# Performance work log

Measured on AMD Instinct MI355X. Metric: run time of the kernel, lower is better.

## Reference

```python
import jax, jax.numpy as jnp
import numpy as np

N_HEAD, D_MODEL, D_K, D_V = 16, 1024, 64, 64
B, LQ, LK = 4, 2048, 2048


def setup_inputs() -> dict:
    key = jax.random.key(0)
    ks = jax.random.split(key, 10)
    q = jax.random.normal(ks[0], (B, LQ, D_MODEL), dtype=jnp.float32)
    k = jax.random.normal(ks[1], (B, LK, D_MODEL), dtype=jnp.float32)
    v = jax.random.normal(ks[2], (B, LK, D_MODEL), dtype=jnp.float32)
    mask = jax.random.randint(ks[3], (B, LQ, LK), 0, 2).astype(bool)
    s_qk = np.sqrt(2.0 / (D_MODEL + D_K)).astype(np.float32)
    s_v = np.sqrt(2.0 / (D_MODEL + D_V)).astype(np.float32)
    w_qs = jax.random.normal(ks[4], (D_MODEL, N_HEAD * D_K), dtype=jnp.float32) * s_qk
    w_ks = jax.random.normal(ks[5], (D_MODEL, N_HEAD * D_K), dtype=jnp.float32) * s_qk
    w_vs = jax.random.normal(ks[6], (D_MODEL, N_HEAD * D_V), dtype=jnp.float32) * s_v
    b_qs = jnp.zeros((N_HEAD * D_K,), jnp.float32)
    b_ks = jnp.zeros((N_HEAD * D_K,), jnp.float32)
    b_vs = jnp.zeros((N_HEAD * D_V,), jnp.float32)
    fc_w = jax.random.normal(ks[7], (N_HEAD * D_V, D_MODEL), dtype=jnp.float32) * np.sqrt(2.0 / (N_HEAD * D_V + D_MODEL)).astype(np.float32)
    fc_b = jnp.zeros((D_MODEL,), jnp.float32)
    return {"q": q, "k": k, "v": v, "mask": mask,
            "w_qs": w_qs, "b_qs": b_qs, "w_ks": w_ks, "b_ks": b_ks,
            "w_vs": w_vs, "b_vs": b_vs, "fc_w": fc_w, "fc_b": fc_b}


def mha(q, k, v, mask, w_qs, b_qs, w_ks, b_ks, w_vs, b_vs, fc_w, fc_b):
    residual = q
    b, lq, _ = q.shape
    lk = k.shape[1]
    # project and split heads: [b, h, len, d]
    qh = (q @ w_qs + b_qs).reshape(b, lq, N_HEAD, D_K).transpose(0, 2, 1, 3)
    kh = (k @ w_ks + b_ks).reshape(b, lk, N_HEAD, D_K).transpose(0, 2, 1, 3)
    vh = (v @ w_vs + b_vs).reshape(b, lk, N_HEAD, D_V).transpose(0, 2, 1, 3)
    temperature = jnp.asarray(D_K ** 0.5, qh.dtype)
    attn = jnp.einsum('bhqd,bhkd->bhqk', qh, kh) / temperature
    attn = jnp.where(mask[:, None, :, :], -jnp.inf, attn)
    attn = jax.nn.softmax(attn, axis=-1)  # dropout is identity in eval
    out = jnp.einsum('bhqk,bhkd->bhqd', attn, vh)
    out = out.transpose(0, 2, 1, 3).reshape(b, lq, N_HEAD * D_V)
    out = out @ fc_w + fc_b
    return out + residual, attn


def reference(q, k, v, mask, w_qs, b_qs, w_ks, b_ks, w_vs, b_vs, fc_w, fc_b):
    return mha(q, k, v, mask, w_qs, b_qs, w_ks, b_ks, w_vs, b_vs, fc_w, fc_b)
```

## Files before the change

### kernel.cpp

```cpp
#include <hip/hip_runtime.h>
#include <cstdint>
#include <cstddef>

typedef unsigned short u16;
typedef __bf16 bf16x8 __attribute__((ext_vector_type(8)));
typedef float floatx4 __attribute__((ext_vector_type(4)));
typedef u16 u16x8 __attribute__((ext_vector_type(8)));

#define NHEAD 16
#define DHEAD 64
#define BATCH 4
#define SEQ 2048
#define DMODEL 1024

__device__ __forceinline__ u16 f2b(float f) {
  union { float f; unsigned u; } x; x.f = f;
  unsigned r = x.u + 0x7fffu + ((x.u >> 16) & 1u);
  return (u16)(r >> 16);
}

__device__ __forceinline__ floatx4 mfma16(bf16x8 a, bf16x8 b, floatx4 c) {
  return __builtin_amdgcn_mfma_f32_16x16x32_bf16(a, b, c, 0, 0, 0);
}

__global__ __launch_bounds__(256) void wtrans(const float* __restrict__ w,
                                              u16* __restrict__ wt) {
  __shared__ u16 tile[64 * 68];
  const int t = threadIdx.x;
  const int d0 = blockIdx.x * 64, c0 = blockIdx.y * 64;
#pragma unroll
  for (int s = 0; s < 4; ++s) {
    int dd = (t >> 4) + s * 16;
    int cc = (t & 15) * 4;
    float4 v = *(const float4*)(w + (size_t)(d0 + dd) * DMODEL + c0 + cc);
    u16* p = &tile[dd * 68 + cc];
    p[0] = f2b(v.x); p[1] = f2b(v.y); p[2] = f2b(v.z); p[3] = f2b(v.w);
  }
  __syncthreads();
#pragma unroll
  for (int s = 0; s < 2; ++s) {
    int cc = (t >> 3) + s * 32;
    int dd = (t & 7) * 8;
    u16x8 rv;
#pragma unroll
    for (int j = 0; j < 8; ++j) rv[j] = tile[(dd + j) * 68 + cc];
    *(u16x8*)(wt + (size_t)(c0 + cc) * DMODEL + d0 + dd) = rv;
  }
}

__global__ __launch_bounds__(256) void gemm128(
    const float* __restrict__ Af, const u16* __restrict__ Ab,
    const u16* __restrict__ WT, const float* __restrict__ bias,
    u16* __restrict__ outb, float* __restrict__ outf,
    const float* __restrict__ resid, int mode) {
  __shared__ __align__(16) u16 sm[2 * 128 * 72];
  u16* sA = sm;
  u16* sB = sm + 128 * 72;
  const int t = threadIdx.x;
  const int w = t >> 6, lane = t & 63, quad = lane >> 4, ln = lane & 15;
  const int Mb = blockIdx.x * 128, Nb = blockIdx.y * 128;
  const int wr = (w >> 1) * 64, wc = (w & 1) * 64;
  floatx4 acc[4][4] = {};
#pragma unroll 1
  for (int kc = 0; kc < 16; ++kc) {
    const int k0 = kc * 64;
    __syncthreads();
    if (mode == 2) {
#pragma unroll
      for (int s = 0; s < 4; ++s) {
        int r = (t >> 3) + s * 32, off = (t & 7) * 8;
        *(u16x8*)(&sA[r * 72 + off]) =
            *(const u16x8*)(Ab + (size_t)(Mb + r) * DMODEL + k0 + off);
      }
    } else {
#pragma unroll
      for (int s = 0; s < 8; ++s) {
        int r = (t >> 4) + s * 16, c = (t & 15) * 4;
        float4 v = *(const float4*)(Af + (size_t)(Mb + r) * DMODEL + k0 + c);
        u16* p = &sA[r * 72 + c];
        p[0] = f2b(v.x); p[1] = f2b(v.y); p[2] = f2b(v.z); p[3] = f2b(v.w);
      }
    }
#pragma unroll
    for (int s = 0; s < 4; ++s) {
      int r = (t >> 3) + s * 32, off = (t & 7) * 8;
      *(u16x8*)(&sB[r * 72 + off]) =
          *(const u16x8*)(WT + (size_t)(Nb + r) * DMODEL + k0 + off);
    }
    __syncthreads();
#pragma unroll
    for (int ks = 0; ks < 2; ++ks) {
      bf16x8 af[4], bfr[4];
#pragma unroll
      for (int m = 0; m < 4; ++m)
        af[m] = *(const bf16x8*)(&sA[(wr + m * 16 + ln) * 72 + quad * 8 + ks * 32]);
#pragma unroll
      for (int n = 0; n < 4; ++n)
        bfr[n] = *(const bf16x8*)(&sB[(wc + n * 16 + ln) * 72 + quad * 8 + ks * 32]);
#pragma unroll
      for (int m = 0; m < 4; ++m)
#pragma unroll
        for (int n = 0; n < 4; ++n)
          acc[m][n] = mfma16(af[m], bfr[n], acc[m][n]);
    }
  }
  float bv[4];
#pragma unroll
  for (int n = 0; n < 4; ++n) bv[n] = bias[Nb + wc + n * 16 + ln];

  if (mode == 0) {
#pragma unroll
    for (int m = 0; m < 4; ++m)
#pragma unroll
      for (int n = 0; n < 4; ++n)
#pragma unroll
        for (int rr = 0; rr < 4; ++rr) {
          int row = Mb + wr + m * 16 + quad * 4 + rr;
          int c = Nb + wc + n * 16 + ln;
          int bi = row >> 11, lq = row & 2047, h = c >> 6, dk = c & 63;
          outb[(((size_t)bi * NHEAD + h) * SEQ + lq) * DHEAD + dk] =
              f2b(acc[m][n][rr] + bv[n]);
        }
  } else if (mode == 2) {
#pragma unroll
    for (int m = 0; m < 4; ++m)
#pragma unroll
      for (int n = 0; n < 4; ++n)
#pragma unroll
        for (int rr = 0; rr < 4; ++rr) {
          int row = Mb + wr + m * 16 + quad * 4 + rr;
          int c = Nb + wc + n * 16 + ln;
          size_t idx = (size_t)row * DMODEL + c;
          outf[idx] = acc[m][n][rr] + bv[n] + resid[idx];
        }
  } else {
    __syncthreads();
    u16* tb = sm;
#pragma unroll
    for (int m = 0; m < 4; ++m)
#pragma unroll
      for (int n = 0; n < 4; ++n)
#pragma unroll
        for (int rr = 0; rr < 4; ++rr) {
          int rl = wr + m * 16 + quad * 4 + rr;
          int cl = wc + n * 16 + ln;
          tb[rl * 132 + cl] = f2b(acc[m][n][rr] + bv[n]);
        }
    __syncthreads();
    for (int s = 0; s < 64; ++s) {
      int flat = s * 256 + t;
      int cl = flat >> 7, lkl = flat & 127;
      int c = Nb + cl, h = c >> 6, dk = c & 63;
      int lk = Mb + lkl, bi = lk >> 11, lkq = lk & 2047;
      outb[(((size_t)bi * NHEAD + h) * DHEAD + dk) * SEQ + lkq] =
          tb[lkl * 132 + cl];
    }
  }
}

__global__ __launch_bounds__(256) void attn_k(
    const u16* __restrict__ qh, const u16* __restrict__ kh,
    const u16* __restrict__ vT, const void* __restrict__ maskp,
    float* __restrict__ attn_o, u16* __restrict__ ao) {
  __shared__ __align__(16) u16 qs[64 * 72];
  __shared__ __align__(16) u16 ks_[64 * 72];
  __shared__ __align__(16) u16 vs[64 * 72];
  __shared__ __align__(16) u16 ps[64 * 72];
  __shared__ float ms[64], ls[64];
  const int t = threadIdx.x;
  const int w = t >> 6, lane = t & 63, quad = lane >> 4, ln = lane & 15;
  const int qt = blockIdx.x, bh = blockIdx.y;
  const int b = bh >> 4;
  const int q0 = qt * 64;
  const float SC = 0.18033688011112042f;

  unsigned mw = ((const unsigned*)maskp)[lane];
  const bool bytemask = __ballot(mw > 1u) != 0ull;
  const unsigned char* m8 = (const unsigned char*)maskp;
  const unsigned* m32 = (const unsigned*)maskp;
  const size_t mbase = (size_t)b * SEQ * SEQ;

#pragma unroll
  for (int s = 0; s < 2; ++s) {
    int r = (t >> 3) + s * 32, off = (t & 7) * 8;
    *(u16x8*)(&qs[r * 72 + off]) =
        *(const u16x8*)(qh + ((size_t)bh * SEQ + q0 + r) * DHEAD + off);
  }
  float mrun[4], lrun[4];
#pragma unroll
  for (int rr = 0; rr < 4; ++rr) { mrun[rr] = -1e30f; lrun[rr] = 0.f; }

#pragma unroll 1
  for (int kt = 0; kt < 32; ++kt) {
    __syncthreads();
#pragma unroll
    for (int s = 0; s < 2; ++s) {
      int r = (t >> 3) + s * 32, off = (t & 7) * 8;
      *(u16x8*)(&ks_[r * 72 + off]) =
          *(const u16x8*)(kh + ((size_t)bh * SEQ + kt * 64 + r) * DHEAD + off);
    }
    __syncthreads();
    floatx4 sc[4] = {};
#pragma unroll
    for (int kss = 0; kss < 2; ++kss) {
      bf16x8 a = *(const bf16x8*)(&qs[(w * 16 + ln) * 72 + quad * 8 + kss * 32]);
#pragma unroll
      for (int n = 0; n < 4; ++n) {
        bf16x8 bb = *(const bf16x8*)(&ks_[(n * 16 + ln) * 72 + quad * 8 + kss * 32]);
        sc[n] = mfma16(a, bb, sc[n]);
      }
    }
#pragma unroll
    for (int rr = 0; rr < 4; ++rr) {
      int qrow = q0 + w * 16 + quad * 4 + rr;
      float tv[4];
#pragma unroll
      for (int n = 0; n < 4; ++n) {
        int kcol = kt * 64 + n * 16 + ln;
        size_t mi = mbase + (size_t)qrow * SEQ + kcol;
        bool blk = bytemask ? (m8[mi] != 0) : (m32[mi] != 0);
        tv[n] = blk ? -1e30f : sc[n][rr] * SC;
      }
      float cm = fmaxf(fmaxf(tv[0], tv[1]), fmaxf(tv[2], tv[3]));
#pragma unroll
      for (int o = 1; o < 16; o <<= 1) cm = fmaxf(cm, __shfl_xor(cm, o));
      float cs = exp2f(tv[0] - cm) + exp2f(tv[1] - cm) +
                 exp2f(tv[2] - cm) + exp2f(tv[3] - cm);
#pragma unroll
      for (int o = 1; o < 16; o <<= 1) cs += __shfl_xor(cs, o);
      float mnew = fmaxf(mrun[rr], cm);
      lrun[rr] = lrun[rr] * exp2f(mrun[rr] - mnew) + cs * exp2f(cm - mnew);
      mrun[rr] = mnew;
    }
  }
  if (ln == 0) {
#pragma unroll
    for (int rr = 0; rr < 4; ++rr) {
      ms[w * 16 + quad * 4 + rr] = mrun[rr];
      ls[w * 16 + quad * 4 + rr] = lrun[rr];
    }
  }
  __syncthreads();
  float mf[4], il[4];
#pragma unroll
  for (int rr = 0; rr < 4; ++rr) {
    mf[rr] = ms[w * 16 + quad * 4 + rr];
    il[rr] = 1.0f / ls[w * 16 + quad * 4 + rr];
  }

  floatx4 oa[4] = {};
#pragma unroll 1
  for (int kt = 0; kt < 32; ++kt) {
    __syncthreads();
#pragma unroll
    for (int s = 0; s < 2; ++s) {
      int r = (t >> 3) + s * 32, off = (t & 7) * 8;
      *(u16x8*)(&ks_[r * 72 + off]) =
          *(const u16x8*)(kh + ((size_t)bh * SEQ + kt * 64 + r) * DHEAD + off);
      *(u16x8*)(&vs[r * 72 + off]) =
          *(const u16x8*)(vT + ((size_t)bh * DHEAD + r) * SEQ + kt * 64 + off);
    }
    __syncthreads();
    floatx4 sc[4] = {};
#pragma unroll
    for (int kss = 0; kss < 2; ++kss) {
      bf16x8 a = *(const bf16x8*)(&qs[(w * 16 + ln) * 72 + quad * 8 + kss * 32]);
#pragma unroll
      for (int n = 0; n < 4; ++n) {
        bf16x8 bb = *(const bf16x8*)(&ks_[(n * 16 + ln) * 72 + quad * 8 + kss * 32]);
        sc[n] = mfma16(a, bb, sc[n]);
      }
    }
#pragma unroll
    for (int rr = 0; rr < 4; ++rr) {
      int qrow = q0 + w * 16 + quad * 4 + rr;
#pragma unroll
      for (int n = 0; n < 4; ++n) {
        int kcol = kt * 64 + n * 16 + ln;
        size_t mi = mbase + (size_t)qrow * SEQ + kcol;
        bool blk = bytemask ? (m8[mi] != 0) : (m32[mi] != 0);
        float tvv = blk ? -1e30f : sc[n][rr] * SC;
        float pn = exp2f(tvv - mf[rr]) * il[rr];
        attn_o[(size_t)bh * SEQ * SEQ + (size_t)qrow * SEQ + kcol] = pn;
        ps[(w * 16 + quad * 4 + rr) * 72 + n * 16 + ln] = f2b(pn);
      }
    }
    __syncthreads();
#pragma unroll
    for (int kss = 0; kss < 2; ++kss) {
      bf16x8 a = *(const bf16x8*)(&ps[(w * 16 + ln) * 72 + quad * 8 + kss * 32]);
#pragma unroll
      for (int n = 0; n < 4; ++n) {
        bf16x8 bb = *(const bf16x8*)(&vs[(n * 16 + ln) * 72 + quad * 8 + kss * 32]);
        oa[n] = mfma16(a, bb, oa[n]);
      }
    }
  }
#pragma unroll
  for (int n = 0; n < 4; ++n)
#pragma unroll
    for (int rr = 0; rr < 4; ++rr) {
      int row = q0 + w * 16 + quad * 4 + rr;
      ao[((size_t)b * SEQ + row) * DMODEL + (bh & 15) * DHEAD + n * 16 + ln] =
          f2b(oa[n][rr]);
    }
}

extern "C" void kernel_launch(void* const* d_in, const int* in_sizes, int n_in,
                              void* d_out, int out_size, void* d_ws,
                              size_t ws_size, hipStream_t stream) {
  (void)in_sizes; (void)n_in; (void)out_size; (void)ws_size;
  const float* q = (const float*)d_in[0];
  const float* k = (const float*)d_in[1];
  const float* v = (const float*)d_in[2];
  const void* mask = d_in[3];
  const float* w_qs = (const float*)d_in[4];
  const float* b_qs = (const float*)d_in[5];
  const float* w_ks = (const float*)d_in[6];
  const float* b_ks = (const float*)d_in[7];
  const float* w_vs = (const float*)d_in[8];
  const float* b_vs = (const float*)d_in[9];
  const float* fc_w = (const float*)d_in[10];
  const float* fc_b = (const float*)d_in[11];

  char* ws = (char*)d_ws;
  const size_t WSZ = (size_t)DMODEL * DMODEL * 2;
  const size_t HSZ = (size_t)BATCH * NHEAD * SEQ * DHEAD * 2;
  u16* wqT = (u16*)(ws + 0 * WSZ);
  u16* wkT = (u16*)(ws + 1 * WSZ);
  u16* wvT = (u16*)(ws + 2 * WSZ);
  u16* fcT = (u16*)(ws + 3 * WSZ);
  u16* qh = (u16*)(ws + 4 * WSZ);
  u16* kh = (u16*)(ws + 4 * WSZ + HSZ);
  u16* vhT = (u16*)(ws + 4 * WSZ + 2 * HSZ);
  u16* ao = (u16*)(ws + 4 * WSZ + 3 * HSZ);

  float* out0 = (float*)d_out;
  float* attn = out0 + (size_t)BATCH * SEQ * DMODEL;

  dim3 tgrid(16, 16);
  wtrans<<<tgrid, 256, 0, stream>>>(w_qs, wqT);
  wtrans<<<tgrid, 256, 0, stream>>>(w_ks, wkT);
  wtrans<<<tgrid, 256, 0, stream>>>(w_vs, wvT);
  wtrans<<<tgrid, 256, 0, stream>>>(fc_w, fcT);

  dim3 ggrid(64, 8);
  gemm128<<<ggrid, 256, 0, stream>>>(q, nullptr, wqT, b_qs, qh, nullptr, nullptr, 0);
  gemm128<<<ggrid, 256, 0, stream>>>(k, nullptr, wkT, b_ks, kh, nullptr, nullptr, 0);
  gemm128<<<ggrid, 256, 0, stream>>>(v, nullptr, wvT, b_vs, vhT, nullptr, nullptr, 1);

  attn_k<<<dim3(32, 64), 256, 0, stream>>>(qh, kh, vhT, mask, attn, ao);

  gemm128<<<ggrid, 256, 0, stream>>>(nullptr, ao, fcT, fc_b, nullptr, out0, q, 2);
}
```

Before: 2.251 ms.

## Bit-pack attention mask and rework attention kernel without LDS staging or running max

A new pre-pass packs the boolean mask into 64-bit words per row and 64-key tile, so the attention kernel reads one word per row per tile instead of gathering individual mask bytes or ints. The attention kernel keeps Q fragments in registers and loads K and V fragments straight from global memory per wave. This removes the shared-memory staging and the block-wide barriers, leaving each wave only a private P buffer. It also drops the running-max rescaling and exponentiates scaled scores directly, and writes attention probabilities with nontemporal stores. The trade-offs are that softmax without max subtraction can overflow for large scores, and that K/V reuse now depends on the cache rather than on shared memory.

```diff
diff --git a/kernel.cpp b/kernel.cpp
--- a/kernel.cpp
+++ b/kernel.cpp
@@ -3,6 +3,7 @@
 #include <cstddef>
 
 typedef unsigned short u16;
+typedef unsigned long long u64;
 typedef __bf16 bf16x8 __attribute__((ext_vector_type(8)));
 typedef float floatx4 __attribute__((ext_vector_type(4)));
 typedef u16 u16x8 __attribute__((ext_vector_type(8)));
@@ -46,6 +47,43 @@
     for (int j = 0; j < 8; ++j) rv[j] = tile[(dd + j) * 68 + cc];
     *(u16x8*)(wt + (size_t)(c0 + cc) * DMODEL + d0 + dd) = rv;
   }
+}
+
+__global__ __launch_bounds__(256) void maskpack(const void* __restrict__ maskp,
+                                                u64* __restrict__ mpk) {
+  const int t = threadIdx.x;
+  unsigned mw = ((const unsigned*)maskp)[t & 63];
+  const bool bytemask = __ballot(mw > 1u) != 0ull;
+  const int rl = t >> 5, kt = t & 31;
+  const int row = blockIdx.x * 8 + rl;
+  const int b = blockIdx.y;
+  const size_t eoff = ((size_t)b * SEQ + row) * SEQ + (size_t)kt * 64;
+  u64 bits = 0;
+  if (bytemask) {
+    const uint4* p = (const uint4*)((const unsigned char*)maskp + eoff);
+#pragma unroll
+    for (int j = 0; j < 4; ++j) {
+      uint4 v = p[j];
+      unsigned wd[4] = {v.x, v.y, v.z, v.w};
+#pragma unroll
+      for (int q = 0; q < 4; ++q)
+#pragma unroll
+        for (int by = 0; by < 4; ++by)
+          bits |= (u64)(((wd[q] >> (8 * by)) & 0xffu) ? 1u : 0u)
+                  << (j * 16 + q * 4 + by);
+    }
+  } else {
+    const uint4* p = (const uint4*)((const unsigned*)maskp + eoff);
+#pragma unroll
+    for (int j = 0; j < 16; ++j) {
+      uint4 v = p[j];
+      bits |= (u64)(v.x ? 1 : 0) << (j * 4 + 0);
+      bits |= (u64)(v.y ? 1 : 0) << (j * 4 + 1);
+      bits |= (u64)(v.z ? 1 : 0) << (j * 4 + 2);
+      bits |= (u64)(v.w ? 1 : 0) << (j * 4 + 3);
+    }
+  }
+  mpk[((size_t)b * SEQ + row) * 32 + kt] = bits;
 }
 
 __global__ __launch_bounds__(256) void gemm128(
@@ -158,149 +196,107 @@
   }
 }
 
-__global__ __launch_bounds__(256) void attn_k(
+__global__ __launch_bounds__(256, 4) void attn2(
     const u16* __restrict__ qh, const u16* __restrict__ kh,
-    const u16* __restrict__ vT, const void* __restrict__ maskp,
+    const u16* __restrict__ vT, const u64* __restrict__ mpk,
     float* __restrict__ attn_o, u16* __restrict__ ao) {
-  __shared__ __align__(16) u16 qs[64 * 72];
-  __shared__ __align__(16) u16 ks_[64 * 72];
-  __shared__ __align__(16) u16 vs[64 * 72];
-  __shared__ __align__(16) u16 ps[64 * 72];
-  __shared__ float ms[64], ls[64];
+  __shared__ __align__(16) u16 ps[4][16 * 72];
   const int t = threadIdx.x;
   const int w = t >> 6, lane = t & 63, quad = lane >> 4, ln = lane & 15;
   const int qt = blockIdx.x, bh = blockIdx.y;
   const int b = bh >> 4;
-  const int q0 = qt * 64;
+  const int q0 = qt * 64 + w * 16;
   const float SC = 0.18033688011112042f;
 
-  unsigned mw = ((const unsigned*)maskp)[lane];
-  const bool bytemask = __ballot(mw > 1u) != 0ull;
-  const unsigned char* m8 = (const unsigned char*)maskp;
-  const unsigned* m32 = (const unsigned*)maskp;
-  const size_t mbase = (size_t)b * SEQ * SEQ;
-
-#pragma unroll
-  for (int s = 0; s < 2; ++s) {
-    int r = (t >> 3) + s * 32, off = (t & 7) * 8;
-    *(u16x8*)(&qs[r * 72 + off]) =
-        *(const u16x8*)(qh + ((size_t)bh * SEQ + q0 + r) * DHEAD + off);
-  }
-  float mrun[4], lrun[4];
-#pragma unroll
-  for (int rr = 0; rr < 4; ++rr) { mrun[rr] = -1e30f; lrun[rr] = 0.f; }
-
+  bf16x8 qf[2];
+  {
+    const u16* qbase = qh + ((size_t)bh * SEQ + q0 + ln) * DHEAD + quad * 8;
+    qf[0] = *(const bf16x8*)(qbase);
+    qf[1] = *(const bf16x8*)(qbase + 32);
+  }
+  const u16* kbase = kh + (size_t)bh * SEQ * DHEAD;
+  const u16* vbase = vT + (size_t)bh * DHEAD * SEQ;
+  const u64* mrow = mpk + ((size_t)b * SEQ + q0 + quad * 4) * 32;
+
+  float lsum[4] = {0.f, 0.f, 0.f, 0.f};
 #pragma unroll 1
   for (int kt = 0; kt < 32; ++kt) {
-    __syncthreads();
-#pragma unroll
-    for (int s = 0; s < 2; ++s) {
-      int r = (t >> 3) + s * 32, off = (t & 7) * 8;
-      *(u16x8*)(&ks_[r * 72 + off]) =
-          *(const u16x8*)(kh + ((size_t)bh * SEQ + kt * 64 + r) * DHEAD + off);
-    }
-    __syncthreads();
-    floatx4 sc[4] = {};
-#pragma unroll
-    for (int kss = 0; kss < 2; ++kss) {
-      bf16x8 a = *(const bf16x8*)(&qs[(w * 16 + ln) * 72 + quad * 8 + kss * 32]);
-#pragma unroll
-      for (int n = 0; n < 4; ++n) {
-        bf16x8 bb = *(const bf16x8*)(&ks_[(n * 16 + ln) * 72 + quad * 8 + kss * 32]);
-        sc[n] = mfma16(a, bb, sc[n]);
-      }
-    }
+    u64 mv[4];
+#pragma unroll
+    for (int rr = 0; rr < 4; ++rr) mv[rr] = mrow[rr * 32 + kt];
+    floatx4 sc4[4] = {};
+#pragma unroll
+    for (int kss = 0; kss < 2; ++kss)
+#pragma unroll
+      for (int n = 0; n < 4; ++n) {
+        bf16x8 kf = *(const bf16x8*)(kbase + (size_t)(kt * 64 + n * 16 + ln) * DHEAD +
+                                     quad * 8 + kss * 32);
+        sc4[n] = mfma16(qf[kss], kf, sc4[n]);
+      }
 #pragma unroll
     for (int rr = 0; rr < 4; ++rr) {
-      int qrow = q0 + w * 16 + quad * 4 + rr;
-      float tv[4];
-#pragma unroll
-      for (int n = 0; n < 4; ++n) {
-        int kcol = kt * 64 + n * 16 + ln;
-        size_t mi = mbase + (size_t)qrow * SEQ + kcol;
-        bool blk = bytemask ? (m8[mi] != 0) : (m32[mi] != 0);
-        tv[n] = blk ? -1e30f : sc[n][rr] * SC;
-      }
-      float cm = fmaxf(fmaxf(tv[0], tv[1]), fmaxf(tv[2], tv[3]));
-#pragma unroll
-      for (int o = 1; o < 16; o <<= 1) cm = fmaxf(cm, __shfl_xor(cm, o));
-      float cs = exp2f(tv[0] - cm) + exp2f(tv[1] - cm) +
-                 exp2f(tv[2] - cm) + exp2f(tv[3] - cm);
-#pragma unroll
-      for (int o = 1; o < 16; o <<= 1) cs += __shfl_xor(cs, o);
-      float mnew = fmaxf(mrun[rr], cm);
-      lrun[rr] = lrun[rr] * exp2f(mrun[rr] - mnew) + cs * exp2f(cm - mnew);
-      mrun[rr] = mnew;
-    }
-  }
-  if (ln == 0) {
-#pragma unroll
-    for (int rr = 0; rr < 4; ++rr) {
-      ms[w * 16 + quad * 4 + rr] = mrun[rr];
-      ls[w * 16 + quad * 4 + rr] = lrun[rr];
-    }
-  }
-  __syncthreads();
-  float mf[4], il[4];
+#pragma unroll
+      for (int n = 0; n < 4; ++n) {
+        float e = exp2f(sc4[n][rr] * SC);
+        bool blk = (mv[rr] >> (n * 16 + ln)) & 1;
+        lsum[rr] += blk ? 0.f : e;
+      }
+    }
+  }
+  float il[4];
 #pragma unroll
   for (int rr = 0; rr < 4; ++rr) {
-    mf[rr] = ms[w * 16 + quad * 4 + rr];
-    il[rr] = 1.0f / ls[w * 16 + quad * 4 + rr];
+    float s = lsum[rr];
+#pragma unroll
+    for (int o = 1; o < 16; o <<= 1) s += __shfl_xor(s, o);
+    il[rr] = 1.0f / s;
   }
 
   floatx4 oa[4] = {};
+  u16* myps = ps[w];
+  float* pout = attn_o + (size_t)bh * SEQ * SEQ;
 #pragma unroll 1
   for (int kt = 0; kt < 32; ++kt) {
-    __syncthreads();
-#pragma unroll
-    for (int s = 0; s < 2; ++s) {
-      int r = (t >> 3) + s * 32, off = (t & 7) * 8;
-      *(u16x8*)(&ks_[r * 72 + off]) =
-          *(const u16x8*)(kh + ((size_t)bh * SEQ + kt * 64 + r) * DHEAD + off);
-      *(u16x8*)(&vs[r * 72 + off]) =
-          *(const u16x8*)(vT + ((size_t)bh * DHEAD + r) * SEQ + kt * 64 + off);
-    }
-    __syncthreads();
-    floatx4 sc[4] = {};
+    u64 mv[4];
+#pragma unroll
+    for (int rr = 0; rr < 4; ++rr) mv[rr] = mrow[rr * 32 + kt];
+    floatx4 sc4[4] = {};
+#pragma unroll
+    for (int kss = 0; kss < 2; ++kss)
+#pragma unroll
+      for (int n = 0; n < 4; ++n) {
+        bf16x8 kf = *(const bf16x8*)(kbase + (size_t)(kt * 64 + n * 16 + ln) * DHEAD +
+                                     quad * 8 + kss * 32);
+        sc4[n] = mfma16(qf[kss], kf, sc4[n]);
+      }
+#pragma unroll
+    for (int rr = 0; rr < 4; ++rr) {
+      int qrow = q0 + quad * 4 + rr;
+#pragma unroll
+      for (int n = 0; n < 4; ++n) {
+        bool blk = (mv[rr] >> (n * 16 + ln)) & 1;
+        float pn = blk ? 0.f : exp2f(sc4[n][rr] * SC) * il[rr];
+        __builtin_nontemporal_store(
+            pn, &pout[(size_t)qrow * SEQ + kt * 64 + n * 16 + ln]);
+        myps[(quad * 4 + rr) * 72 + n * 16 + ln] = f2b(pn);
+      }
+    }
 #pragma unroll
     for (int kss = 0; kss < 2; ++kss) {
-      bf16x8 a = *(const bf16x8*)(&qs[(w * 16 + ln) * 72 + quad * 8 + kss * 32]);
-#pragma unroll
-      for (int n = 0; n < 4; ++n) {
-        bf16x8 bb = *(const bf16x8*)(&ks_[(n * 16 + ln) * 72 + quad * 8 + kss * 32]);
-        sc[n] = mfma16(a, bb, sc[n]);
-      }
-    }
+      bf16x8 pa = *(const bf16x8*)(&myps[ln * 72 + quad * 8 + kss * 32]);
+#pragma unroll
+      for (int n = 0; n < 4; ++n) {
+        bf16x8 vf = *(const bf16x8*)(vbase + (size_t)(n * 16 + ln) * SEQ +
+                                     kt * 64 + quad * 8 + kss * 32);
+        oa[n] = mfma16(pa, vf, oa[n]);
+      }
+    }
+  }
+#pragma unroll
+  for (int n = 0; n < 4; ++n)
 #pragma unroll
     for (int rr = 0; rr < 4; ++rr) {
-      int qrow = q0 + w * 16 + quad * 4 + rr;
-#pragma unroll
-      for (int n = 0; n < 4; ++n) {
-        int kcol = kt * 64 + n * 16 + ln;
-        size_t mi = mbase + (size_t)qrow * SEQ + kcol;
-        bool blk = bytemask ? (m8[mi] != 0) : (m32[mi] != 0);
-        float tvv = blk ? -1e30f : sc[n][rr] * SC;
-        float pn = exp2f(tvv - mf[rr]) * il[rr];
-        attn_o[(size_t)bh * SEQ * SEQ + (size_t)qrow * SEQ + kcol] = pn;
-        ps[(w * 16 + quad * 4 + rr) * 72 + n * 16 + ln] = f2b(pn);
-      }
-    }
-    __syncthreads();
-#pragma unroll
-    for (int kss = 0; kss < 2; ++kss) {
-      bf16x8 a = *(const bf16x8*)(&ps[(w * 16 + ln) * 72 + quad * 8 + kss * 32]);
-#pragma unroll
-      for (int n = 0; n < 4; ++n) {
-        bf16x8 bb = *(const bf16x8*)(&vs[(n * 16 + ln) * 72 + quad * 8 + kss * 32]);
-        oa[n] = mfma16(a, bb, oa[n]);
-      }
-    }
-  }
-#pragma unroll
-  for (int n = 0; n < 4; ++n)
-#pragma unroll
-    for (int rr = 0; rr < 4; ++rr) {
-      int row = q0 + w * 16 + quad * 4 + rr;
+      int row = q0 + quad * 4 + rr;
       ao[((size_t)b * SEQ + row) * DMODEL + (bh & 15) * DHEAD + n * 16 + ln] =
           f2b(oa[n][rr]);
     }
@@ -334,6 +330,7 @@
   u16* kh = (u16*)(ws + 4 * WSZ + HSZ);
   u16* vhT = (u16*)(ws + 4 * WSZ + 2 * HSZ);
   u16* ao = (u16*)(ws + 4 * WSZ + 3 * HSZ);
+  u64* mpk = (u64*)(ws + 4 * WSZ + 4 * HSZ);
 
   float* out0 = (float*)d_out;
   float* attn = out0 + (size_t)BATCH * SEQ * DMODEL;
@@ -344,12 +341,14 @@
   wtrans<<<tgrid, 256, 0, stream>>>(w_vs, wvT);
   wtrans<<<tgrid, 256, 0, stream>>>(fc_w, fcT);
 
+  maskpack<<<dim3(SEQ / 8, BATCH), 256, 0, stream>>>(mask, mpk);
+
   dim3 ggrid(64, 8);
   gemm128<<<ggrid, 256, 0, stream>>>(q, nullptr, wqT, b_qs, qh, nullptr, nullptr, 0);
   gemm128<<<ggrid, 256, 0, stream>>>(k, nullptr, wkT, b_ks, kh, nullptr, nullptr, 0);
   gemm128<<<ggrid, 256, 0, stream>>>(v, nullptr, wvT, b_vs, vhT, nullptr, nullptr, 1);
 
-  attn_k<<<dim3(32, 64), 256, 0, stream>>>(qh, kh, vhT, mask, attn, ao);
+  attn2<<<dim3(32, 64), 256, 0, stream>>>(qh, kh, vhT, mpk, attn, ao);
 
   gemm128<<<ggrid, 256, 0, stream>>>(nullptr, ao, fcT, fc_b, nullptr, out0, q, 2);
 }
```

New measurement: 1.923 ms. 14.6% less time.
